# Performance work log

Measured on AMD Instinct MI355X. Metric: run time of the kernel, lower is better.

## Reference

```python
import jax, jax.numpy as jnp
import numpy as np

B, N, C, H, W = 16, 64, 128, 64, 64
IMG = 512.0
SCALE = 0.125          # spatial_scale
MAX_GRID = 16          # >= ceil(max_roi_side * SCALE); boxes built so sides <= 128px -> 16
OUT_CH = 256


def setup_inputs() -> dict:
    key = jax.random.key(0)
    k1, k2, k3, k4, k5 = jax.random.split(key, 5)
    z = jax.random.normal(k1, (B, C, H, W), jnp.float32)
    xy = jax.random.uniform(k2, (B, N, 2), jnp.float32, 0.0, IMG - 128.0)
    wh = jax.random.uniform(k3, (B, N, 2), jnp.float32, 8.0, 128.0)
    bboxes = jnp.concatenate([xy, xy + wh], axis=-1)  # [B,N,4] xyxy, image coords
    W_out = jax.random.normal(k4, (OUT_CH, C), jnp.float32) / np.sqrt(C).astype(np.float32)
    b_out = jax.random.normal(k5, (OUT_CH,), jnp.float32) * 0.01
    return {"z": z, "bboxes": bboxes, "W_out": W_out, "b_out": b_out}


def _prep_coord(c, L):
    # torchvision bilinear edge handling; c: sample coord, L: spatial extent
    inr = (c > -1.0) & (c < float(L))          # out of range -> value 0 (still counted)
    cc = jnp.clip(c, 0.0, None)
    lo = jnp.minimum(jnp.floor(cc).astype(jnp.int32), L - 1)
    hi = jnp.minimum(lo + 1, L - 1)
    cc = jnp.where(lo >= L - 1, lo.astype(c.dtype), cc)
    frac = cc - lo.astype(c.dtype)
    return lo, hi, frac, inr


def roi_align_1x1(z, boxes, scale=SCALE, max_grid=MAX_GRID):
    # z: [B,C,H,W], boxes: [B,N,4] xyxy. torchvision roi_align, output_size=1,
    # aligned=True, sampling_ratio=-1 (adaptive grid = ceil(roi_side), masked to max_grid).
    Bz, Cz, Hh, Ww = z.shape
    b = boxes * scale - 0.5                       # aligned=True offset
    x1, y1, x2, y2 = b[..., 0], b[..., 1], b[..., 2], b[..., 3]
    roi_w, roi_h = x2 - x1, y2 - y1               # [B,N]
    gw = jnp.clip(jnp.ceil(roi_w), 1.0, float(max_grid))
    gh = jnp.clip(jnp.ceil(roi_h), 1.0, float(max_grid))
    g = jnp.arange(max_grid, dtype=z.dtype)
    sy = y1[..., None] + (g + 0.5) * (roi_h / gh)[..., None]   # [B,N,G]
    sx = x1[..., None] + (g + 0.5) * (roi_w / gw)[..., None]
    vy = g < gh[..., None]                        # grid-validity (adaptive count)
    vx = g < gw[..., None]

    yl, yh, fy, iry = _prep_coord(sy, Hh)
    xl, xh, fx, irx = _prep_coord(sx, Ww)
    hy, hx = 1.0 - fy, 1.0 - fx

    zf = z.transpose(0, 2, 3, 1)                  # [B,H,W,C]
    shp = (Bz, boxes.shape[1], max_grid, max_grid)
    Yl = jnp.broadcast_to(yl[..., :, None], shp)
    Yh = jnp.broadcast_to(yh[..., :, None], shp)
    Xl = jnp.broadcast_to(xl[..., None, :], shp)
    Xh = jnp.broadcast_to(xh[..., None, :], shp)

    gather = jax.vmap(lambda zb, yi, xi: zb[yi, xi])   # -> [B,N,G,G,C]
    v11 = gather(zf, Yl, Xl)
    v12 = gather(zf, Yl, Xh)
    v21 = gather(zf, Yh, Xl)
    v22 = gather(zf, Yh, Xh)

    w11 = hy[..., :, None] * hx[..., None, :]
    w12 = hy[..., :, None] * fx[..., None, :]
    w21 = fy[..., :, None] * hx[..., None, :]
    w22 = fy[..., :, None] * fx[..., None, :]
    val = (w11[..., None] * v11 + w12[..., None] * v12
           + w21[..., None] * v21 + w22[..., None] * v22)   # [B,N,G,G,C]

    mask = ((vy[..., :, None] & vx[..., None, :])
            & (iry[..., :, None] & irx[..., None, :])).astype(z.dtype)
    val = val * mask[..., None]
    count = (gh * gw)[..., None]                   # adaptive sample count
    return val.sum(axis=(2, 3)) / count            # [B,N,C]


def reference(z, bboxes, W_out, b_out):
    # roi_align (output 1x1) -> avgpool(1) is identity -> reshape [B,N,C] -> Linear
    feats = roi_align_1x1(z, bboxes)               # [B,N,C]
    return feats @ W_out.T + b_out                 # [B,N,OUT_CH]
```

## Files before the change

kernel.cpp:

```cpp
#include <hip/hip_runtime.h>
#include <hip/hip_bf16.h>

#define B_ 16
#define N_ 64
#define C_ 128
#define H_ 64
#define W_ 64
#define HW_ (H_ * W_)
#define OUT_CH_ 256
#define MAX_GRID_ 16
#define SCALE_ 0.125f

__device__ __forceinline__ unsigned int packbf2(float lo, float hi) {
  __hip_bfloat162 h = __float22bfloat162_rn(float2{lo, hi});
  return *(unsigned int*)&h;
}

__global__ __launch_bounds__(256) void transpose_kernel(
    const float* __restrict__ z, const float* __restrict__ Wm,
    unsigned int* __restrict__ zf, float* __restrict__ Wt) {
  __shared__ unsigned int tile32[128 * 65];
  const int t = threadIdx.x;

  if (blockIdx.y == 16) {
    float* ft = (float*)tile32;
    int x  = blockIdx.x;
    int ot = x & 7, ct = x >> 3;
    int j = t & 31, i0 = t >> 5;
#pragma unroll
    for (int k = 0; k < 4; ++k) {
      int i = i0 + k * 8;
      ft[i * 33 + j] = Wm[(size_t)(ot * 32 + i) * C_ + ct * 32 + j];
    }
    __syncthreads();
#pragma unroll
    for (int k = 0; k < 4; ++k) {
      int i = i0 + k * 8;
      Wt[(size_t)(ct * 32 + i) * OUT_CH_ + ot * 32 + j] = ft[j * 33 + i];
    }
    return;
  }

  const int b  = blockIdx.y;
  const int pt = blockIdx.x;
  const float* zb = z + (size_t)b * C_ * HW_ + pt * 128;
#pragma unroll
  for (int iter = 0; iter < 8; ++iter) {
    int idx = iter * 256 + t;
    int c2  = idx >> 5;
    int p4  = (idx & 31) << 2;
    const float* r0 = zb + (size_t)(c2 * 2) * HW_ + p4;
    float4 a = *(const float4*)r0;
    float4 c = *(const float4*)(r0 + HW_);
    tile32[(p4 + 0) * 65 + c2] = packbf2(a.x, c.x);
    tile32[(p4 + 1) * 65 + c2] = packbf2(a.y, c.y);
    tile32[(p4 + 2) * 65 + c2] = packbf2(a.z, c.z);
    tile32[(p4 + 3) * 65 + c2] = packbf2(a.w, c.w);
  }
  __syncthreads();

  unsigned int* zfb = zf + (size_t)b * HW_ * 64 + (size_t)pt * 128 * 64;
#pragma unroll
  for (int iter = 0; iter < 8; ++iter) {
    int idx = iter * 256 + t;
    int p   = idx >> 4;
    int q   = (idx & 15) << 2;
    uint4 u = *(const uint4*)&tile32[p * 65 + q];
    *(uint4*)(zfb + (size_t)p * 64 + q) = u;
  }
}

__global__ __launch_bounds__(512) void roi_fused_kernel(
    const unsigned int* __restrict__ zf,
    const float* __restrict__ boxes,
    const float* __restrict__ Wt,
    const float* __restrict__ bias,
    float* __restrict__ out)
{
  int bid = blockIdx.x;
  int img = (bid & 7) | ((bid >> 9) << 3);
  int roi = img * N_ + ((bid >> 3) & 63);
  int t   = threadIdx.x;
  int wv  = t >> 6;
  int lane = t & 63;
  int half = lane >> 5;
  int cq   = lane & 31;

  float4 bx = ((const float4*)boxes)[roi];
  float x1 = bx.x * SCALE_ - 0.5f;
  float y1 = bx.y * SCALE_ - 0.5f;
  float roi_w = bx.z * SCALE_ - 0.5f - x1;
  float roi_h = bx.w * SCALE_ - 0.5f - y1;
  float gwf = fminf(fmaxf(ceilf(roi_w), 1.0f), (float)MAX_GRID_);
  float ghf = fminf(fmaxf(ceilf(roi_h), 1.0f), (float)MAX_GRID_);
  int gw = (int)gwf;
  int gh = (int)ghf;
  float stepx = roi_w / gwf;
  float stepy = roi_h / ghf;

  __shared__ float4 xmeta[16];
  __shared__ float4 ymeta[16];
  if (t < 16) {
    int g = t;
    float sx = x1 + ((float)g + 0.5f) * stepx;
    float v  = (g < gw && sx > -1.0f && sx < (float)W_) ? 1.0f : 0.0f;
    float cx = fmaxf(sx, 0.0f);
    int xl = (int)cx;
    xl = xl < (W_ - 1) ? xl : (W_ - 1);
    int xh = (xl + 1) < (W_ - 1) ? (xl + 1) : (W_ - 1);
    if (xl >= W_ - 1) cx = (float)xl;
    float fx = cx - (float)xl;
    float4 m;
    m.x = __int_as_float(xl << 6);
    m.y = __int_as_float(xh << 6);
    m.z = (1.0f - fx) * v;
    m.w = fx * v;
    xmeta[g] = m;
  } else if (t >= 64 && t < 80) {
    int g = t - 64;
    float sy = y1 + ((float)g + 0.5f) * stepy;
    float v  = (g < gh && sy > -1.0f && sy < (float)H_) ? 1.0f : 0.0f;
    float cy = fmaxf(sy, 0.0f);
    int yl = (int)cy;
    yl = yl < (H_ - 1) ? yl : (H_ - 1);
    int yh = (yl + 1) < (H_ - 1) ? (yl + 1) : (H_ - 1);
    if (yl >= H_ - 1) cy = (float)yl;
    float fy = cy - (float)yl;
    float4 m;
    m.x = __int_as_float(yl * (W_ * 64));
    m.y = __int_as_float(yh * (W_ * 64));
    m.z = (1.0f - fy) * v;
    m.w = fy * v;
    ymeta[g] = m;
  }
  __syncthreads();

  const unsigned int* zb = zf + (size_t)img * (HW_ * 64) + (cq << 1);

  float a0 = 0.0f, a1 = 0.0f, a2 = 0.0f, a3 = 0.0f;
  for (int gy = wv; gy < gh; gy += 8) {
    float4 ym = ymeta[gy];
    int yloff = __float_as_int(ym.x);
    int yhoff = __float_as_int(ym.y);
    float ah = ym.z, af = ym.w;

    for (int gxp = 0; gxp < gw; gxp += 2) {
      int gx = gxp + half;
      float4 xm = xmeta[gx];
      int xloff = __float_as_int(xm.x);
      int xhoff = __float_as_int(xm.y);
      float w11 = ah * xm.z, w12 = ah * xm.w;
      float w21 = af * xm.z, w22 = af * xm.w;

      uint2 v11 = *(const uint2*)(zb + yloff + xloff);
      uint2 v12 = *(const uint2*)(zb + yloff + xhoff);
      uint2 v21 = *(const uint2*)(zb + yhoff + xloff);
      uint2 v22 = *(const uint2*)(zb + yhoff + xhoff);

      a0 += w11 * __uint_as_float(v11.x << 16)
          + w12 * __uint_as_float(v12.x << 16)
          + w21 * __uint_as_float(v21.x << 16)
          + w22 * __uint_as_float(v22.x << 16);
      a1 += w11 * __uint_as_float(v11.x & 0xffff0000u)
          + w12 * __uint_as_float(v12.x & 0xffff0000u)
          + w21 * __uint_as_float(v21.x & 0xffff0000u)
          + w22 * __uint_as_float(v22.x & 0xffff0000u);
      a2 += w11 * __uint_as_float(v11.y << 16)
          + w12 * __uint_as_float(v12.y << 16)
          + w21 * __uint_as_float(v21.y << 16)
          + w22 * __uint_as_float(v22.y << 16);
      a3 += w11 * __uint_as_float(v11.y & 0xffff0000u)
          + w12 * __uint_as_float(v12.y & 0xffff0000u)
          + w21 * __uint_as_float(v21.y & 0xffff0000u)
          + w22 * __uint_as_float(v22.y & 0xffff0000u);
    }
  }

  __shared__ float red[16][128];
  __shared__ float feat[128];
  __shared__ float lin[2][256];
  *(float4*)&red[wv * 2 + half][cq << 2] = float4{a0, a1, a2, a3};
  __syncthreads();
  if (t < 128) {
    float s = 0.0f;
#pragma unroll
    for (int r = 0; r < 16; ++r) s += red[r][t];
    feat[t] = s * (1.0f / (ghf * gwf));
  }
  __syncthreads();

  int oc = t & 255;
  int hk = t >> 8;
  const float* wp = Wt + (size_t)(hk * 64) * OUT_CH_ + oc;
  const float* fp = feat + hk * 64;
  float a = 0.0f;
#pragma unroll 8
  for (int k = 0; k < 64; ++k)
    a += fp[k] * wp[(size_t)k * OUT_CH_];
  lin[hk][oc] = a;
  __syncthreads();
  if (t < 256)
    out[(size_t)roi * OUT_CH_ + t] = lin[0][t] + lin[1][t] + bias[t];
}

extern "C" void kernel_launch(void* const* d_in, const int* in_sizes, int n_in,
                              void* d_out, int out_size, void* d_ws, size_t ws_size,
                              hipStream_t stream) {
  const float* z     = (const float*)d_in[0];
  const float* boxes = (const float*)d_in[1];
  const float* Wm    = (const float*)d_in[2];
  const float* bias  = (const float*)d_in[3];
  float* out = (float*)d_out;

  char* ws = (char*)d_ws;
  unsigned int* zf = (unsigned int*)ws;
  float* Wt = (float*)(ws + (size_t)B_ * HW_ * C_ * 2);

  transpose_kernel<<<dim3(HW_ / 128, B_ + 1), 256, 0, stream>>>(z, Wm, zf, Wt);
  roi_fused_kernel<<<B_ * N_, 512, 0, stream>>>(zf, boxes, Wt, bias, out);
}
```

Baseline: 97.01 us.

## Process two ROIs per block to amortize linear weight loads

Each block now handles two ROIs from the same image. It computes metadata for both, runs the bilinear accumulation for each in turn, and then does the linear layer with each half of the threads serving one ROI over all 128 input channels. This halves the grid, so each Wt row is read by half as many blocks, and the block setup is amortized over two ROIs. In exchange each block does serial work for two ROIs and the grid drops to 512 blocks, which may underfill the GPU's compute units.

Result: no change. 96.86 us (-0.2%).

```diff
diff --git a/kernel.cpp b/kernel.cpp
--- a/kernel.cpp
+++ b/kernel.cpp
@@ -77,130 +77,147 @@
     const float* __restrict__ bias,
     float* __restrict__ out)
 {
-  int bid = blockIdx.x;
-  int img = (bid & 7) | ((bid >> 9) << 3);
-  int roi = img * N_ + ((bid >> 3) & 63);
-  int t   = threadIdx.x;
-  int wv  = t >> 6;
+  int bid  = blockIdx.x;
+  int xcd  = bid & 7;
+  int slot = bid >> 3;
+  int img  = xcd | ((slot >> 5) << 3);
+  int pr   = slot & 31;
+  int roi0 = img * N_ + pr * 2;
+
+  int t    = threadIdx.x;
+  int wv   = t >> 6;
   int lane = t & 63;
   int half = lane >> 5;
   int cq   = lane & 31;
 
-  float4 bx = ((const float4*)boxes)[roi];
-  float x1 = bx.x * SCALE_ - 0.5f;
-  float y1 = bx.y * SCALE_ - 0.5f;
-  float roi_w = bx.z * SCALE_ - 0.5f - x1;
-  float roi_h = bx.w * SCALE_ - 0.5f - y1;
-  float gwf = fminf(fmaxf(ceilf(roi_w), 1.0f), (float)MAX_GRID_);
-  float ghf = fminf(fmaxf(ceilf(roi_h), 1.0f), (float)MAX_GRID_);
-  int gw = (int)gwf;
-  int gh = (int)ghf;
-  float stepx = roi_w / gwf;
-  float stepy = roi_h / ghf;
-
-  __shared__ float4 xmeta[16];
-  __shared__ float4 ymeta[16];
-  if (t < 16) {
-    int g = t;
-    float sx = x1 + ((float)g + 0.5f) * stepx;
-    float v  = (g < gw && sx > -1.0f && sx < (float)W_) ? 1.0f : 0.0f;
-    float cx = fmaxf(sx, 0.0f);
-    int xl = (int)cx;
-    xl = xl < (W_ - 1) ? xl : (W_ - 1);
-    int xh = (xl + 1) < (W_ - 1) ? (xl + 1) : (W_ - 1);
-    if (xl >= W_ - 1) cx = (float)xl;
-    float fx = cx - (float)xl;
-    float4 m;
-    m.x = __int_as_float(xl << 6);
-    m.y = __int_as_float(xh << 6);
-    m.z = (1.0f - fx) * v;
-    m.w = fx * v;
-    xmeta[g] = m;
-  } else if (t >= 64 && t < 80) {
-    int g = t - 64;
-    float sy = y1 + ((float)g + 0.5f) * stepy;
-    float v  = (g < gh && sy > -1.0f && sy < (float)H_) ? 1.0f : 0.0f;
-    float cy = fmaxf(sy, 0.0f);
-    int yl = (int)cy;
-    yl = yl < (H_ - 1) ? yl : (H_ - 1);
-    int yh = (yl + 1) < (H_ - 1) ? (yl + 1) : (H_ - 1);
-    if (yl >= H_ - 1) cy = (float)yl;
-    float fy = cy - (float)yl;
-    float4 m;
-    m.x = __int_as_float(yl * (W_ * 64));
-    m.y = __int_as_float(yh * (W_ * 64));
-    m.z = (1.0f - fy) * v;
-    m.w = fy * v;
-    ymeta[g] = m;
+  __shared__ float4 xmeta[2][16];
+  __shared__ float4 ymeta[2][16];
+  __shared__ float  cnt_inv[2];
+  __shared__ int    dims[2][2];
+
+  if (t < 32 || (t >= 64 && t < 96)) {
+    int isY = t >> 6;
+    int tt  = t & 31;
+    int r   = tt >> 4;
+    int g   = tt & 15;
+    float4 bx = ((const float4*)boxes)[roi0 + r];
+    float x1 = bx.x * SCALE_ - 0.5f;
+    float y1 = bx.y * SCALE_ - 0.5f;
+    float roi_w = bx.z * SCALE_ - 0.5f - x1;
+    float roi_h = bx.w * SCALE_ - 0.5f - y1;
+    float gwf = fminf(fmaxf(ceilf(roi_w), 1.0f), (float)MAX_GRID_);
+    float ghf = fminf(fmaxf(ceilf(roi_h), 1.0f), (float)MAX_GRID_);
+    if (!isY) {
+      int gw = (int)gwf;
+      float stepx = roi_w / gwf;
+      float sx = x1 + ((float)g + 0.5f) * stepx;
+      float v  = (g < gw && sx > -1.0f && sx < (float)W_) ? 1.0f : 0.0f;
+      float cx = fmaxf(sx, 0.0f);
+      int xl = (int)cx;
+      xl = xl < (W_ - 1) ? xl : (W_ - 1);
+      int xh = (xl + 1) < (W_ - 1) ? (xl + 1) : (W_ - 1);
+      if (xl >= W_ - 1) cx = (float)xl;
+      float fx = cx - (float)xl;
+      float4 m;
+      m.x = __int_as_float(xl << 6);
+      m.y = __int_as_float(xh << 6);
+      m.z = (1.0f - fx) * v;
+      m.w = fx * v;
+      xmeta[r][g] = m;
+      if (g == 0) {
+        dims[r][0] = gw;
+        cnt_inv[r] = 1.0f / (ghf * gwf);
+      }
+    } else {
+      int gh = (int)ghf;
+      float stepy = roi_h / ghf;
+      float sy = y1 + ((float)g + 0.5f) * stepy;
+      float v  = (g < gh && sy > -1.0f && sy < (float)H_) ? 1.0f : 0.0f;
+      float cy = fmaxf(sy, 0.0f);
+      int yl = (int)cy;
+      yl = yl < (H_ - 1) ? yl : (H_ - 1);
+      int yh = (yl + 1) < (H_ - 1) ? (yl + 1) : (H_ - 1);
+      if (yl >= H_ - 1) cy = (float)yl;
+      float fy = cy - (float)yl;
+      float4 m;
+      m.x = __int_as_float(yl * (W_ * 64));
+      m.y = __int_as_float(yh * (W_ * 64));
+      m.z = (1.0f - fy) * v;
+      m.w = fy * v;
+      ymeta[r][g] = m;
+      if (g == 0) dims[r][1] = gh;
+    }
   }
   __syncthreads();
 
   const unsigned int* zb = zf + (size_t)img * (HW_ * 64) + (cq << 1);
 
-  float a0 = 0.0f, a1 = 0.0f, a2 = 0.0f, a3 = 0.0f;
-  for (int gy = wv; gy < gh; gy += 8) {
-    float4 ym = ymeta[gy];
-    int yloff = __float_as_int(ym.x);
-    int yhoff = __float_as_int(ym.y);
-    float ah = ym.z, af = ym.w;
-
-    for (int gxp = 0; gxp < gw; gxp += 2) {
-      int gx = gxp + half;
-      float4 xm = xmeta[gx];
-      int xloff = __float_as_int(xm.x);
-      int xhoff = __float_as_int(xm.y);
-      float w11 = ah * xm.z, w12 = ah * xm.w;
-      float w21 = af * xm.z, w22 = af * xm.w;
-
-      uint2 v11 = *(const uint2*)(zb + yloff + xloff);
-      uint2 v12 = *(const uint2*)(zb + yloff + xhoff);
-      uint2 v21 = *(const uint2*)(zb + yhoff + xloff);
-      uint2 v22 = *(const uint2*)(zb + yhoff + xhoff);
-
-      a0 += w11 * __uint_as_float(v11.x << 16)
-          + w12 * __uint_as_float(v12.x << 16)
-          + w21 * __uint_as_float(v21.x << 16)
-          + w22 * __uint_as_float(v22.x << 16);
-      a1 += w11 * __uint_as_float(v11.x & 0xffff0000u)
-          + w12 * __uint_as_float(v12.x & 0xffff0000u)
-          + w21 * __uint_as_float(v21.x & 0xffff0000u)
-          + w22 * __uint_as_float(v22.x & 0xffff0000u);
-      a2 += w11 * __uint_as_float(v11.y << 16)
-          + w12 * __uint_as_float(v12.y << 16)
-          + w21 * __uint_as_float(v21.y << 16)
-          + w22 * __uint_as_float(v22.y << 16);
-      a3 += w11 * __uint_as_float(v11.y & 0xffff0000u)
-          + w12 * __uint_as_float(v12.y & 0xffff0000u)
-          + w21 * __uint_as_float(v21.y & 0xffff0000u)
-          + w22 * __uint_as_float(v22.y & 0xffff0000u);
-    }
-  }
-
-  __shared__ float red[16][128];
-  __shared__ float feat[128];
-  __shared__ float lin[2][256];
-  *(float4*)&red[wv * 2 + half][cq << 2] = float4{a0, a1, a2, a3};
-  __syncthreads();
-  if (t < 128) {
+  __shared__ float red[2][16][128];
+  __shared__ float feat[2][128];
+
+#pragma unroll
+  for (int r = 0; r < 2; ++r) {
+    int gw = dims[r][0];
+    int gh = dims[r][1];
+    float a0 = 0.0f, a1 = 0.0f, a2 = 0.0f, a3 = 0.0f;
+    for (int gy = wv; gy < gh; gy += 8) {
+      float4 ym = ymeta[r][gy];
+      int yloff = __float_as_int(ym.x);
+      int yhoff = __float_as_int(ym.y);
+      float ah = ym.z, af = ym.w;
+
+      for (int gxp = 0; gxp < gw; gxp += 2) {
+        int gx = gxp + half;
+        float4 xm = xmeta[r][gx];
+        int xloff = __float_as_int(xm.x);
+        int xhoff = __float_as_int(xm.y);
+        float w11 = ah * xm.z, w12 = ah * xm.w;
+        float w21 = af * xm.z, w22 = af * xm.w;
+
+        uint2 v11 = *(const uint2*)(zb + yloff + xloff);
+        uint2 v12 = *(const uint2*)(zb + yloff + xhoff);
+        uint2 v21 = *(const uint2*)(zb + yhoff + xloff);
+        uint2 v22 = *(const uint2*)(zb + yhoff + xhoff);
+
+        a0 += w11 * __uint_as_float(v11.x << 16)
+            + w12 * __uint_as_float(v12.x << 16)
+            + w21 * __uint_as_float(v21.x << 16)
+            + w22 * __uint_as_float(v22.x << 16);
+        a1 += w11 * __uint_as_float(v11.x & 0xffff0000u)
+            + w12 * __uint_as_float(v12.x & 0xffff0000u)
+            + w21 * __uint_as_float(v21.x & 0xffff0000u)
+            + w22 * __uint_as_float(v22.x & 0xffff0000u);
+        a2 += w11 * __uint_as_float(v11.y << 16)
+            + w12 * __uint_as_float(v12.y << 16)
+            + w21 * __uint_as_float(v21.y << 16)
+            + w22 * __uint_as_float(v22.y << 16);
+        a3 += w11 * __uint_as_float(v11.y & 0xffff0000u)
+            + w12 * __uint_as_float(v12.y & 0xffff0000u)
+            + w21 * __uint_as_float(v21.y & 0xffff0000u)
+            + w22 * __uint_as_float(v22.y & 0xffff0000u);
+      }
+    }
+    *(float4*)&red[r][wv * 2 + half][cq << 2] = float4{a0, a1, a2, a3};
+  }
+  __syncthreads();
+
+  if (t < 256) {
+    int r = t >> 7, c = t & 127;
     float s = 0.0f;
 #pragma unroll
-    for (int r = 0; r < 16; ++r) s += red[r][t];
-    feat[t] = s * (1.0f / (ghf * gwf));
+    for (int j = 0; j < 16; ++j) s += red[r][j][c];
+    feat[r][c] = s * cnt_inv[r];
   }
   __syncthreads();
 
   int oc = t & 255;
-  int hk = t >> 8;
-  const float* wp = Wt + (size_t)(hk * 64) * OUT_CH_ + oc;
-  const float* fp = feat + hk * 64;
-  float a = 0.0f;
+  int r  = t >> 8;
+  const float* fp = feat[r];
+  float a = bias[oc];
 #pragma unroll 8
-  for (int k = 0; k < 64; ++k)
-    a += fp[k] * wp[(size_t)k * OUT_CH_];
-  lin[hk][oc] = a;
-  __syncthreads();
-  if (t < 256)
-    out[(size_t)roi * OUT_CH_ + t] = lin[0][t] + lin[1][t] + bias[t];
+  for (int k = 0; k < C_; ++k)
+    a += fp[k] * Wt[(size_t)k * OUT_CH_ + oc];
+  out[(size_t)(roi0 + r) * OUT_CH_ + oc] = a;
 }
 
 extern "C" void kernel_launch(void* const* d_in, const int* in_sizes, int n_in,
@@ -217,5 +234,5 @@
   float* Wt = (float*)(ws + (size_t)B_ * HW_ * C_ * 2);
 
   transpose_kernel<<<dim3(HW_ / 128, B_ + 1), 256, 0, stream>>>(z, Wm, zf, Wt);
-  roi_fused_kernel<<<B_ * N_, 512, 0, stream>>>(zf, boxes, Wt, bias, out);
-}
+  roi_fused_kernel<<<B_ * N_ / 2, 512, 0, stream>>>(zf, boxes, Wt, bias, out);
+}
```

## Fuse transpose and ROI kernels into one cooperative kernel with atomic work queue

Applied to the files above, without the earlier changes.

Merges the bf16 channel-last transpose and the ROI-align-plus-linear kernel into one cooperative launch of 512 blocks, separated by a grid-wide sync. After the sync, blocks pull ROIs dynamically from per-image-group atomic counters to balance uneven ROI sizes. This removes a kernel launch boundary and tail effects. In exchange it adds a grid barrier, atomic contention, and a dependency on every block being co-resident under cooperative launch.

After: 174.6 us. 1.8x slower.

```diff
diff --git a/kernel.cpp b/kernel.cpp
--- a/kernel.cpp
+++ b/kernel.cpp
@@ -1,5 +1,6 @@
 #include <hip/hip_runtime.h>
 #include <hip/hip_bf16.h>
+#include <hip/hip_cooperative_groups.h>
 
 #define B_ 16
 #define N_ 64
@@ -11,196 +12,203 @@
 #define MAX_GRID_ 16
 #define SCALE_ 0.125f
 
+namespace cg = cooperative_groups;
+
 __device__ __forceinline__ unsigned int packbf2(float lo, float hi) {
   __hip_bfloat162 h = __float22bfloat162_rn(float2{lo, hi});
   return *(unsigned int*)&h;
 }
 
-__global__ __launch_bounds__(256) void transpose_kernel(
-    const float* __restrict__ z, const float* __restrict__ Wm,
-    unsigned int* __restrict__ zf, float* __restrict__ Wt) {
-  __shared__ unsigned int tile32[128 * 65];
-  const int t = threadIdx.x;
-
-  if (blockIdx.y == 16) {
-    float* ft = (float*)tile32;
-    int x  = blockIdx.x;
-    int ot = x & 7, ct = x >> 3;
-    int j = t & 31, i0 = t >> 5;
-#pragma unroll
-    for (int k = 0; k < 4; ++k) {
-      int i = i0 + k * 8;
-      ft[i * 33 + j] = Wm[(size_t)(ot * 32 + i) * C_ + ct * 32 + j];
-    }
-    __syncthreads();
-#pragma unroll
-    for (int k = 0; k < 4; ++k) {
-      int i = i0 + k * 8;
-      Wt[(size_t)(ct * 32 + i) * OUT_CH_ + ot * 32 + j] = ft[j * 33 + i];
-    }
-    return;
+__global__ __launch_bounds__(512, 4) void fused_all(
+    const float* __restrict__ z, const float* __restrict__ boxes,
+    const float* __restrict__ Wm, const float* __restrict__ bias,
+    unsigned int* __restrict__ zf, float* __restrict__ Wt,
+    int* __restrict__ ctr, float* __restrict__ out)
+{
+  __shared__ __align__(16) char smem[128 * 65 * 4];
+  const int t   = threadIdx.x;
+  const int bid = blockIdx.x;
+
+  {
+    unsigned int* tile32 = (unsigned int*)smem;
+    int b = bid >> 5, pt = bid & 31;
+    const float* zb = z + (size_t)b * C_ * HW_ + pt * 128;
+#pragma unroll
+    for (int iter = 0; iter < 4; ++iter) {
+      int idx = iter * 512 + t;
+      int c2  = idx >> 5;
+      int p4  = (idx & 31) << 2;
+      const float* r0 = zb + (size_t)(c2 * 2) * HW_ + p4;
+      float4 a = *(const float4*)r0;
+      float4 c = *(const float4*)(r0 + HW_);
+      tile32[(p4 + 0) * 65 + c2] = packbf2(a.x, c.x);
+      tile32[(p4 + 1) * 65 + c2] = packbf2(a.y, c.y);
+      tile32[(p4 + 2) * 65 + c2] = packbf2(a.z, c.z);
+      tile32[(p4 + 3) * 65 + c2] = packbf2(a.w, c.w);
+    }
+    __syncthreads();
+    unsigned int* zfb = zf + (size_t)b * HW_ * 64 + (size_t)pt * 128 * 64;
+#pragma unroll
+    for (int iter = 0; iter < 4; ++iter) {
+      int idx = iter * 512 + t;
+      int p   = idx >> 4;
+      int q   = (idx & 15) << 2;
+      *(uint4*)(zfb + (size_t)p * 64 + q) = *(const uint4*)&tile32[p * 65 + q];
+    }
+    if (bid < 8) {
+      if (t < 256) {
+        int oc = bid * 32 + (t >> 3);
+        int cs = (t & 7) * 16;
+#pragma unroll
+        for (int k = 0; k < 16; ++k)
+          Wt[(size_t)(cs + k) * OUT_CH_ + oc] = Wm[(size_t)oc * C_ + cs + k];
+      }
+      if (t == 511) ctr[bid] = 0;
+    }
   }
 
-  const int b  = blockIdx.y;
-  const int pt = blockIdx.x;
-  const float* zb = z + (size_t)b * C_ * HW_ + pt * 128;
-#pragma unroll
-  for (int iter = 0; iter < 8; ++iter) {
-    int idx = iter * 256 + t;
-    int c2  = idx >> 5;
-    int p4  = (idx & 31) << 2;
-    const float* r0 = zb + (size_t)(c2 * 2) * HW_ + p4;
-    float4 a = *(const float4*)r0;
-    float4 c = *(const float4*)(r0 + HW_);
-    tile32[(p4 + 0) * 65 + c2] = packbf2(a.x, c.x);
-    tile32[(p4 + 1) * 65 + c2] = packbf2(a.y, c.y);
-    tile32[(p4 + 2) * 65 + c2] = packbf2(a.z, c.z);
-    tile32[(p4 + 3) * 65 + c2] = packbf2(a.w, c.w);
+  cg::this_grid().sync();
+
+  float4* xmeta = (float4*)smem;
+  float4* ymeta = (float4*)(smem + 256);
+  float*  s_cnt = (float*)(smem + 512);
+  int*    s_gw  = (int*)(smem + 516);
+  int*    s_gh  = (int*)(smem + 520);
+  int*    s_g   = (int*)(smem + 768);
+  float (*red)[128] = (float(*)[128])(smem + 1024);
+  float*  feat  = (float*)(smem + 9216);
+  float*  lin   = (float*)(smem + 9728);
+
+  const int myq  = bid & 7;
+  const int wv   = t >> 6;
+  const int lane = t & 63;
+  const int half = lane >> 5;
+  const int cq   = lane & 31;
+
+  for (;;) {
+    __syncthreads();
+    if (t == 0) *s_g = atomicAdd(&ctr[myq], 1);
+    __syncthreads();
+    int g = *s_g;
+    if (g >= 2 * N_) break;
+    int img = myq + ((g >> 6) << 3);
+    int roi = img * N_ + (g & 63);
+
+    if (t < 16 || (t >= 64 && t < 80)) {
+      int isY = t >> 6;
+      int gg  = t & 15;
+      float4 bx = ((const float4*)boxes)[roi];
+      float x1 = bx.x * SCALE_ - 0.5f;
+      float y1 = bx.y * SCALE_ - 0.5f;
+      float roi_w = bx.z * SCALE_ - 0.5f - x1;
+      float roi_h = bx.w * SCALE_ - 0.5f - y1;
+      float gwf = fminf(fmaxf(ceilf(roi_w), 1.0f), (float)MAX_GRID_);
+      float ghf = fminf(fmaxf(ceilf(roi_h), 1.0f), (float)MAX_GRID_);
+      if (!isY) {
+        int gw = (int)gwf;
+        float stepx = roi_w / gwf;
+        float sx = x1 + ((float)gg + 0.5f) * stepx;
+        float v  = (gg < gw && sx > -1.0f && sx < (float)W_) ? 1.0f : 0.0f;
+        float cx = fmaxf(sx, 0.0f);
+        int xl = (int)cx;
+        xl = xl < (W_ - 1) ? xl : (W_ - 1);
+        int xh = (xl + 1) < (W_ - 1) ? (xl + 1) : (W_ - 1);
+        if (xl >= W_ - 1) cx = (float)xl;
+        float fx = cx - (float)xl;
+        float4 m;
+        m.x = __int_as_float(xl << 6);
+        m.y = __int_as_float(xh << 6);
+        m.z = (1.0f - fx) * v;
+        m.w = fx * v;
+        xmeta[gg] = m;
+        if (gg == 0) { *s_gw = gw; *s_cnt = 1.0f / (ghf * gwf); }
+      } else {
+        int gh = (int)ghf;
+        float stepy = roi_h / ghf;
+        float sy = y1 + ((float)gg + 0.5f) * stepy;
+        float v  = (gg < gh && sy > -1.0f && sy < (float)H_) ? 1.0f : 0.0f;
+        float cy = fmaxf(sy, 0.0f);
+        int yl = (int)cy;
+        yl = yl < (H_ - 1) ? yl : (H_ - 1);
+        int yh = (yl + 1) < (H_ - 1) ? (yl + 1) : (H_ - 1);
+        if (yl >= H_ - 1) cy = (float)yl;
+        float fy = cy - (float)yl;
+        float4 m;
+        m.x = __int_as_float(yl * (W_ * 64));
+        m.y = __int_as_float(yh * (W_ * 64));
+        m.z = (1.0f - fy) * v;
+        m.w = fy * v;
+        ymeta[gg] = m;
+        if (gg == 0) *s_gh = gh;
+      }
+    }
+    __syncthreads();
+
+    int gw = *s_gw, gh = *s_gh;
+    float cnt_inv = *s_cnt;
+    const unsigned int* zb = zf + (size_t)img * (HW_ * 64) + (cq << 1);
+
+    float a0 = 0.0f, a1 = 0.0f, a2 = 0.0f, a3 = 0.0f;
+    for (int gy = wv; gy < gh; gy += 8) {
+      float4 ym = ymeta[gy];
+      int yloff = __float_as_int(ym.x);
+      int yhoff = __float_as_int(ym.y);
+      float ah = ym.z, af = ym.w;
+      for (int gxp = 0; gxp < gw; gxp += 2) {
+        int gx = gxp + half;
+        float4 xm = xmeta[gx];
+        int xloff = __float_as_int(xm.x);
+        int xhoff = __float_as_int(xm.y);
+        float w11 = ah * xm.z, w12 = ah * xm.w;
+        float w21 = af * xm.z, w22 = af * xm.w;
+
+        uint2 v11 = *(const uint2*)(zb + yloff + xloff);
+        uint2 v12 = *(const uint2*)(zb + yloff + xhoff);
+        uint2 v21 = *(const uint2*)(zb + yhoff + xloff);
+        uint2 v22 = *(const uint2*)(zb + yhoff + xhoff);
+
+        a0 += w11 * __uint_as_float(v11.x << 16)
+            + w12 * __uint_as_float(v12.x << 16)
+            + w21 * __uint_as_float(v21.x << 16)
+            + w22 * __uint_as_float(v22.x << 16);
+        a1 += w11 * __uint_as_float(v11.x & 0xffff0000u)
+            + w12 * __uint_as_float(v12.x & 0xffff0000u)
+            + w21 * __uint_as_float(v21.x & 0xffff0000u)
+            + w22 * __uint_as_float(v22.x & 0xffff0000u);
+        a2 += w11 * __uint_as_float(v11.y << 16)
+            + w12 * __uint_as_float(v12.y << 16)
+            + w21 * __uint_as_float(v21.y << 16)
+            + w22 * __uint_as_float(v22.y << 16);
+        a3 += w11 * __uint_as_float(v11.y & 0xffff0000u)
+            + w12 * __uint_as_float(v12.y & 0xffff0000u)
+            + w21 * __uint_as_float(v21.y & 0xffff0000u)
+            + w22 * __uint_as_float(v22.y & 0xffff0000u);
+      }
+    }
+    *(float4*)&red[wv * 2 + half][cq << 2] = float4{a0, a1, a2, a3};
+    __syncthreads();
+
+    if (t < 128) {
+      float s = 0.0f;
+#pragma unroll
+      for (int j = 0; j < 16; ++j) s += red[j][t];
+      feat[t] = s * cnt_inv;
+    }
+    __syncthreads();
+
+    int oc = t & 255;
+    int hk = t >> 8;
+    const float* wp = Wt + (size_t)(hk * 64) * OUT_CH_ + oc;
+    const float* fp = feat + hk * 64;
+    float a = 0.0f;
+#pragma unroll 8
+    for (int k = 0; k < 64; ++k)
+      a += fp[k] * wp[(size_t)k * OUT_CH_];
+    lin[hk * 256 + oc] = a;
+    __syncthreads();
+    if (t < 256)
+      out[(size_t)roi * OUT_CH_ + t] = lin[t] + lin[256 + t] + bias[t];
   }
-  __syncthreads();
-
-  unsigned int* zfb = zf + (size_t)b * HW_ * 64 + (size_t)pt * 128 * 64;
-#pragma unroll
-  for (int iter = 0; iter < 8; ++iter) {
-    int idx = iter * 256 + t;
-    int p   = idx >> 4;
-    int q   = (idx & 15) << 2;
-    uint4 u = *(const uint4*)&tile32[p * 65 + q];
-    *(uint4*)(zfb + (size_t)p * 64 + q) = u;
-  }
-}
-
-__global__ __launch_bounds__(512) void roi_fused_kernel(
-    const unsigned int* __restrict__ zf,
-    const float* __restrict__ boxes,
-    const float* __restrict__ Wt,
-    const float* __restrict__ bias,
-    float* __restrict__ out)
-{
-  int bid = blockIdx.x;
-  int img = (bid & 7) | ((bid >> 9) << 3);
-  int roi = img * N_ + ((bid >> 3) & 63);
-  int t   = threadIdx.x;
-  int wv  = t >> 6;
-  int lane = t & 63;
-  int half = lane >> 5;
-  int cq   = lane & 31;
-
-  float4 bx = ((const float4*)boxes)[roi];
-  float x1 = bx.x * SCALE_ - 0.5f;
-  float y1 = bx.y * SCALE_ - 0.5f;
-  float roi_w = bx.z * SCALE_ - 0.5f - x1;
-  float roi_h = bx.w * SCALE_ - 0.5f - y1;
-  float gwf = fminf(fmaxf(ceilf(roi_w), 1.0f), (float)MAX_GRID_);
-  float ghf = fminf(fmaxf(ceilf(roi_h), 1.0f), (float)MAX_GRID_);
-  int gw = (int)gwf;
-  int gh = (int)ghf;
-  float stepx = roi_w / gwf;
-  float stepy = roi_h / ghf;
-
-  __shared__ float4 xmeta[16];
-  __shared__ float4 ymeta[16];
-  if (t < 16) {
-    int g = t;
-    float sx = x1 + ((float)g + 0.5f) * stepx;
-    float v  = (g < gw && sx > -1.0f && sx < (float)W_) ? 1.0f : 0.0f;
-    float cx = fmaxf(sx, 0.0f);
-    int xl = (int)cx;
-    xl = xl < (W_ - 1) ? xl : (W_ - 1);
-    int xh = (xl + 1) < (W_ - 1) ? (xl + 1) : (W_ - 1);
-    if (xl >= W_ - 1) cx = (float)xl;
-    float fx = cx - (float)xl;
-    float4 m;
-    m.x = __int_as_float(xl << 6);
-    m.y = __int_as_float(xh << 6);
-    m.z = (1.0f - fx) * v;
-    m.w = fx * v;
-    xmeta[g] = m;
-  } else if (t >= 64 && t < 80) {
-    int g = t - 64;
-    float sy = y1 + ((float)g + 0.5f) * stepy;
-    float v  = (g < gh && sy > -1.0f && sy < (float)H_) ? 1.0f : 0.0f;
-    float cy = fmaxf(sy, 0.0f);
-    int yl = (int)cy;
-    yl = yl < (H_ - 1) ? yl : (H_ - 1);
-    int yh = (yl + 1) < (H_ - 1) ? (yl + 1) : (H_ - 1);
-    if (yl >= H_ - 1) cy = (float)yl;
-    float fy = cy - (float)yl;
-    float4 m;
-    m.x = __int_as_float(yl * (W_ * 64));
-    m.y = __int_as_float(yh * (W_ * 64));
-    m.z = (1.0f - fy) * v;
-    m.w = fy * v;
-    ymeta[g] = m;
-  }
-  __syncthreads();
-
-  const unsigned int* zb = zf + (size_t)img * (HW_ * 64) + (cq << 1);
-
-  float a0 = 0.0f, a1 = 0.0f, a2 = 0.0f, a3 = 0.0f;
-  for (int gy = wv; gy < gh; gy += 8) {
-    float4 ym = ymeta[gy];
-    int yloff = __float_as_int(ym.x);
-    int yhoff = __float_as_int(ym.y);
-    float ah = ym.z, af = ym.w;
-
-    for (int gxp = 0; gxp < gw; gxp += 2) {
-      int gx = gxp + half;
-      float4 xm = xmeta[gx];
-      int xloff = __float_as_int(xm.x);
-      int xhoff = __float_as_int(xm.y);
-      float w11 = ah * xm.z, w12 = ah * xm.w;
-      float w21 = af * xm.z, w22 = af * xm.w;
-
-      uint2 v11 = *(const uint2*)(zb + yloff + xloff);
-      uint2 v12 = *(const uint2*)(zb + yloff + xhoff);
-      uint2 v21 = *(const uint2*)(zb + yhoff + xloff);
-      uint2 v22 = *(const uint2*)(zb + yhoff + xhoff);
-
-      a0 += w11 * __uint_as_float(v11.x << 16)
-          + w12 * __uint_as_float(v12.x << 16)
-          + w21 * __uint_as_float(v21.x << 16)
-          + w22 * __uint_as_float(v22.x << 16);
-      a1 += w11 * __uint_as_float(v11.x & 0xffff0000u)
-          + w12 * __uint_as_float(v12.x & 0xffff0000u)
-          + w21 * __uint_as_float(v21.x & 0xffff0000u)
-          + w22 * __uint_as_float(v22.x & 0xffff0000u);
-      a2 += w11 * __uint_as_float(v11.y << 16)
-          + w12 * __uint_as_float(v12.y << 16)
-          + w21 * __uint_as_float(v21.y << 16)
-          + w22 * __uint_as_float(v22.y << 16);
-      a3 += w11 * __uint_as_float(v11.y & 0xffff0000u)
-          + w12 * __uint_as_float(v12.y & 0xffff0000u)
-          + w21 * __uint_as_float(v21.y & 0xffff0000u)
-          + w22 * __uint_as_float(v22.y & 0xffff0000u);
-    }
-  }
-
-  __shared__ float red[16][128];
-  __shared__ float feat[128];
-  __shared__ float lin[2][256];
-  *(float4*)&red[wv * 2 + half][cq << 2] = float4{a0, a1, a2, a3};
-  __syncthreads();
-  if (t < 128) {
-    float s = 0.0f;
-#pragma unroll
-    for (int r = 0; r < 16; ++r) s += red[r][t];
-    feat[t] = s * (1.0f / (ghf * gwf));
-  }
-  __syncthreads();
-
-  int oc = t & 255;
-  int hk = t >> 8;
-  const float* wp = Wt + (size_t)(hk * 64) * OUT_CH_ + oc;
-  const float* fp = feat + hk * 64;
-  float a = 0.0f;
-#pragma unroll 8
-  for (int k = 0; k < 64; ++k)
-    a += fp[k] * wp[(size_t)k * OUT_CH_];
-  lin[hk][oc] = a;
-  __syncthreads();
-  if (t < 256)
-    out[(size_t)roi * OUT_CH_ + t] = lin[0][t] + lin[1][t] + bias[t];
 }
 
 extern "C" void kernel_launch(void* const* d_in, const int* in_sizes, int n_in,
@@ -215,7 +223,10 @@
   char* ws = (char*)d_ws;
   unsigned int* zf = (unsigned int*)ws;
   float* Wt = (float*)(ws + (size_t)B_ * HW_ * C_ * 2);
-
-  transpose_kernel<<<dim3(HW_ / 128, B_ + 1), 256, 0, stream>>>(z, Wm, zf, Wt);
-  roi_fused_kernel<<<B_ * N_, 512, 0, stream>>>(zf, boxes, Wt, bias, out);
+  int*  ctr = (int*)(ws + (size_t)B_ * HW_ * C_ * 2 + C_ * OUT_CH_ * 4);
+
+  void* args[] = {(void*)&z, (void*)&boxes, (void*)&Wm, (void*)&bias,
+                  (void*)&zf, (void*)&Wt, (void*)&ctr, (void*)&out};
+  hipLaunchCooperativeKernel((const void*)fused_all, dim3(512), dim3(512),
+                             args, 0, stream);
 }
```
